# Kernel tuning notes

Hardware: AMD Instinct MI355X
Metric: run time of the kernel (lower is better)

## Reference

```python
import jax, jax.numpy as jnp
import numpy as np

B, S, D, H = 1, 2048, 1280, 16
HD = D // H  # 80


def setup_inputs() -> dict:
    key = jax.random.key(0)
    ks = jax.random.split(key, 6)
    return {
        "hidden_states": jax.random.normal(ks[0], (B, S, D), dtype=jnp.float32),
        "rotary_pos_emb": jax.random.normal(ks[1], (S, HD // 2), dtype=jnp.float32),
        "qkv_w": jax.random.normal(ks[2], (3 * D, D), dtype=jnp.float32) * 0.02,
        "qkv_b": jax.random.normal(ks[3], (3 * D,), dtype=jnp.float32) * 0.02,
        "proj_w": jax.random.normal(ks[4], (D, D), dtype=jnp.float32) * 0.02,
        "proj_b": jax.random.normal(ks[5], (D,), dtype=jnp.float32) * 0.02,
    }


def reference(hidden_states, rotary_pos_emb, qkv_w, qkv_b, proj_w, proj_b):
    b, s, d = hidden_states.shape
    h = H
    hd = d // h
    scaling = hd ** -0.5

    # fused QKV projection: [b, s, 3*d]
    qkv = hidden_states @ qkv_w.T + qkv_b
    qkv = qkv.reshape(b, s, 3, h, hd)
    q, k, v = qkv[:, :, 0], qkv[:, :, 1], qkv[:, :, 2]  # each [b, s, h, hd]

    # rotary embedding: cos/sin [s, hd//2] -> [1, s, 1, hd]
    cos = jnp.cos(rotary_pos_emb)
    sin = jnp.sin(rotary_pos_emb)
    cos = jnp.concatenate([cos, cos], axis=-1)[None, :, None, :]
    sin = jnp.concatenate([sin, sin], axis=-1)[None, :, None, :]

    def apply_rope(x):
        x1, x2 = x[..., : hd // 2], x[..., hd // 2:]
        return x * cos + jnp.concatenate([-x2, x1], axis=-1) * sin

    q = apply_rope(q)
    k = apply_rope(k)

    # [b, h, s, hd]
    q = q.transpose(0, 2, 1, 3)
    k = k.transpose(0, 2, 1, 3)
    v = v.transpose(0, 2, 1, 3)

    # naive full attention matrix [b, h, s, s]
    attn = jnp.einsum("bhqd,bhkd->bhqk", q, k) * scaling
    attn = jax.nn.softmax(attn, axis=-1)
    out = jnp.einsum("bhqk,bhkd->bhqd", attn, v)
    out = out.transpose(0, 2, 1, 3).reshape(b, s, d)
    return out @ proj_w.T + proj_b
```

## Files before the change

kernel.cpp:

```cpp
#include <hip/hip_runtime.h>
#include <math.h>

#define SS 2048
#define DD 1280
#define HH 16
#define HDD 80
#define ND3 3840

typedef __attribute__((ext_vector_type(8))) short short8;
typedef __attribute__((ext_vector_type(4))) short s16x4;
typedef __attribute__((ext_vector_type(4))) float f32x4;
typedef __attribute__((ext_vector_type(8))) _Float16 h16x8;
typedef __attribute__((ext_vector_type(4))) _Float16 h16x4;

__device__ inline short f2bf(float f) {
    union { float f; unsigned u; } x; x.f = f;
    unsigned r = x.u + 0x7FFF + ((x.u >> 16) & 1);
    return (short)(r >> 16);
}

__global__ __launch_bounds__(256) void split_f16(
    const float* __restrict__ a, _Float16* __restrict__ ah, int nbA,
    const float* __restrict__ b, _Float16* __restrict__ bh, int nbB,
    const float* __restrict__ c, _Float16* __restrict__ ch)
{
    const float* x; _Float16* h;
    int blk = blockIdx.x;
    if (blk < nbA)            { x = a; h = ah; }
    else if (blk < nbA + nbB) { blk -= nbA; x = b; h = bh; }
    else                      { blk -= nbA + nbB; x = c; h = ch; }
    int i = (blk * 256 + threadIdx.x) * 4;
    float4 v = *(const float4*)(x + i);
    h16x4 hv;
    hv[0] = (_Float16)v.x; hv[1] = (_Float16)v.y;
    hv[2] = (_Float16)v.z; hv[3] = (_Float16)v.w;
    *(h16x4*)(h + i) = hv;
}

#define LDSA(m, kg) ((m) * 32 + (((kg) ^ (((m) >> 1) & 3)) << 3))

template <int BMT, int BNT>
__global__ __launch_bounds__(256) void gemm_f16_sk(
    const _Float16* __restrict__ Ah, const _Float16* __restrict__ Bh,
    const float* __restrict__ bias, _Float16* __restrict__ Cp,
    int M, int N, int K, int Kh)
{
    constexpr int IT = BMT / 32;
    constexpr int JT = BNT / 32;
    constexpr int AU = BMT / 64;
    constexpr int BU = BNT / 64;
    __shared__ _Float16 AhS[BMT * 32];
    __shared__ _Float16 BhS[BNT * 32];

    const int tid = threadIdx.x;
    const int w = tid >> 6;
    const int lane = tid & 63;
    const int l15 = lane & 15;
    const int quad = lane >> 4;
    const int wm = w >> 1, wn = w & 1;
    const int bm = blockIdx.y * BMT;
    const int bn = blockIdx.x * BNT;
    const int z = blockIdx.z;
    const int kbeg = z * Kh, kend = kbeg + Kh;

    f32x4 acc[IT][JT];
    #pragma unroll
    for (int i = 0; i < IT; ++i)
        #pragma unroll
        for (int j = 0; j < JT; ++j)
            acc[i][j] = (f32x4){0.f, 0.f, 0.f, 0.f};

    h16x8 rah[AU], rbh[BU];
    auto loadg = [&](int k0) {
        #pragma unroll
        for (int u = 0; u < AU; ++u) {
            int c = tid + u * 256, m = c >> 2, kg = c & 3;
            rah[u] = *(const h16x8*)(Ah + (size_t)(bm + m) * K + k0 + kg * 8);
        }
        #pragma unroll
        for (int u = 0; u < BU; ++u) {
            int c = tid + u * 256, m = c >> 2, kg = c & 3;
            rbh[u] = *(const h16x8*)(Bh + (size_t)(bn + m) * K + k0 + kg * 8);
        }
    };

    loadg(kbeg);
    for (int k0 = kbeg; k0 < kend; k0 += 32) {
        __syncthreads();
        #pragma unroll
        for (int u = 0; u < AU; ++u) {
            int c = tid + u * 256, m = c >> 2, kg = c & 3;
            *(h16x8*)&AhS[LDSA(m, kg)] = rah[u];
        }
        #pragma unroll
        for (int u = 0; u < BU; ++u) {
            int c = tid + u * 256, m = c >> 2, kg = c & 3;
            *(h16x8*)&BhS[LDSA(m, kg)] = rbh[u];
        }
        __syncthreads();
        if (k0 + 32 < kend) loadg(k0 + 32);

        h16x8 af[IT], bf[JT];
        #pragma unroll
        for (int i = 0; i < IT; ++i) {
            int m = wm * (BMT / 2) + i * 16 + l15;
            af[i] = *(h16x8*)&AhS[LDSA(m, quad)];
        }
        #pragma unroll
        for (int j = 0; j < JT; ++j) {
            int n = wn * (BNT / 2) + j * 16 + l15;
            bf[j] = *(h16x8*)&BhS[LDSA(n, quad)];
        }
        #pragma unroll
        for (int i = 0; i < IT; ++i)
            #pragma unroll
            for (int j = 0; j < JT; ++j)
                acc[i][j] = __builtin_amdgcn_mfma_f32_16x16x32_f16(af[i], bf[j], acc[i][j], 0, 0, 0);
    }

    _Float16* C = Cp + (size_t)z * M * N;
    #pragma unroll
    for (int j = 0; j < JT; ++j) {
        int col = bn + wn * (BNT / 2) + j * 16 + l15;
        float bb = (z == 0) ? bias[col] : 0.f;
        #pragma unroll
        for (int i = 0; i < IT; ++i)
            #pragma unroll
            for (int r = 0; r < 4; ++r) {
                int row = bm + wm * (BMT / 2) + i * 16 + quad * 4 + r;
                C[(size_t)row * N + col] = (_Float16)(acc[i][j][r] + bb);
            }
    }
}

template <int BMT, int BNT>
__global__ __launch_bounds__(256) void gemm_f16(
    const _Float16* __restrict__ Ah, const _Float16* __restrict__ Bh,
    const float* __restrict__ bias, float* __restrict__ C,
    int M, int N, int K)
{
    constexpr int IT = BMT / 32;
    constexpr int JT = BNT / 32;
    constexpr int AU = BMT / 64;
    constexpr int BU = BNT / 64;
    __shared__ _Float16 AhS[BMT * 32];
    __shared__ _Float16 BhS[BNT * 32];

    const int tid = threadIdx.x;
    const int w = tid >> 6;
    const int lane = tid & 63;
    const int l15 = lane & 15;
    const int quad = lane >> 4;
    const int wm = w >> 1, wn = w & 1;
    const int bm = blockIdx.y * BMT;
    const int bn = blockIdx.x * BNT;

    f32x4 acc[IT][JT];
    #pragma unroll
    for (int i = 0; i < IT; ++i)
        #pragma unroll
        for (int j = 0; j < JT; ++j)
            acc[i][j] = (f32x4){0.f, 0.f, 0.f, 0.f};

    h16x8 rah[AU], rbh[BU];
    auto loadg = [&](int k0) {
        #pragma unroll
        for (int u = 0; u < AU; ++u) {
            int c = tid + u * 256, m = c >> 2, kg = c & 3;
            rah[u] = *(const h16x8*)(Ah + (size_t)(bm + m) * K + k0 + kg * 8);
        }
        #pragma unroll
        for (int u = 0; u < BU; ++u) {
            int c = tid + u * 256, m = c >> 2, kg = c & 3;
            rbh[u] = *(const h16x8*)(Bh + (size_t)(bn + m) * K + k0 + kg * 8);
        }
    };

    loadg(0);
    for (int k0 = 0; k0 < K; k0 += 32) {
        __syncthreads();
        #pragma unroll
        for (int u = 0; u < AU; ++u) {
            int c = tid + u * 256, m = c >> 2, kg = c & 3;
            *(h16x8*)&AhS[LDSA(m, kg)] = rah[u];
        }
        #pragma unroll
        for (int u = 0; u < BU; ++u) {
            int c = tid + u * 256, m = c >> 2, kg = c & 3;
            *(h16x8*)&BhS[LDSA(m, kg)] = rbh[u];
        }
        __syncthreads();
        if (k0 + 32 < K) loadg(k0 + 32);

        h16x8 af[IT], bf[JT];
        #pragma unroll
        for (int i = 0; i < IT; ++i) {
            int m = wm * (BMT / 2) + i * 16 + l15;
            af[i] = *(h16x8*)&AhS[LDSA(m, quad)];
        }
        #pragma unroll
        for (int j = 0; j < JT; ++j) {
            int n = wn * (BNT / 2) + j * 16 + l15;
            bf[j] = *(h16x8*)&BhS[LDSA(n, quad)];
        }
        #pragma unroll
        for (int i = 0; i < IT; ++i)
            #pragma unroll
            for (int j = 0; j < JT; ++j)
                acc[i][j] = __builtin_amdgcn_mfma_f32_16x16x32_f16(af[i], bf[j], acc[i][j], 0, 0, 0);
    }

    #pragma unroll
    for (int j = 0; j < JT; ++j) {
        int col = bn + wn * (BNT / 2) + j * 16 + l15;
        float bb = bias[col];
        #pragma unroll
        for (int i = 0; i < IT; ++i)
            #pragma unroll
            for (int r = 0; r < 4; ++r) {
                int row = bm + wm * (BMT / 2) + i * 16 + quad * 4 + r;
                C[(size_t)row * N + col] = acc[i][j][r] + bb;
            }
    }
}

__global__ __launch_bounds__(256) void rope_scatter_bf16(
    const _Float16* __restrict__ p0, const _Float16* __restrict__ p1,
    const float* __restrict__ rpe,
    short* __restrict__ q, short* __restrict__ k, short* __restrict__ v)
{
    __shared__ float cs[40], sn[40];
    const int s = blockIdx.x;
    if (threadIdx.x < 40)
        __sincosf(rpe[s * 40 + threadIdx.x], &sn[threadIdx.x], &cs[threadIdx.x]);
    __syncthreads();
    const float scale = 0.11180339887498949f;
    for (int j = threadIdx.x; j < ND3; j += 256) {
        int p = j / DD;
        int rem = j - p * DD;
        int hh = rem / HDD;
        int d = rem - hh * HDD;
        size_t base = (size_t)s * ND3;
        float x = (float)p0[base + j] + (float)p1[base + j];
        float val;
        if (p == 2) {
            val = x;
        } else {
            int dm = (d < 40) ? d : d - 40;
            size_t oi = base + p * DD + hh * HDD + ((d < 40) ? d + 40 : d - 40);
            float oth = (float)p0[oi] + (float)p1[oi];
            if (d < 40) oth = -oth;
            val = x * cs[dm] + oth * sn[dm];
            if (p == 0) val *= scale;
        }
        short* dst = (p == 0) ? q : (p == 1) ? k : v;
        dst[((size_t)hh * SS + s) * HDD + d] = f2bf(val);
    }
}

__global__ __launch_bounds__(256) void attn_mfma(
    const short* __restrict__ q, const short* __restrict__ k,
    const short* __restrict__ v, _Float16* __restrict__ o_part,
    float* __restrict__ l_part)
{
    __shared__ short Ks[64][88];
    __shared__ short Vts[80 * 64];
    __shared__ short Ps[4][32][72];

    const int h = blockIdx.y;
    const int q0 = blockIdx.x << 7;
    const int z = blockIdx.z;
    const int tid = threadIdx.x;
    const int w = tid >> 6;
    const int lane = tid & 63;
    const int l15 = lane & 15;
    const int quad = lane >> 4;

    const short* qbase = q + (size_t)h * SS * HDD;
    const short* kbase = k + (size_t)h * SS * HDD;
    const short* vbase = v + (size_t)h * SS * HDD;

    short8 qf[2][3];
    #pragma unroll
    for (int i = 0; i < 2; ++i) {
        const int row = q0 + w * 32 + i * 16 + l15;
        qf[i][0] = *(const short8*)(qbase + (size_t)row * HDD + quad * 8);
        qf[i][1] = *(const short8*)(qbase + (size_t)row * HDD + 32 + quad * 8);
        qf[i][2] = (quad < 2) ? *(const short8*)(qbase + (size_t)row * HDD + 64 + quad * 8)
                              : (short8)0;
    }

    if (tid < 64)
        *(short8*)&Ks[tid][80] = (short8)0;

    float lsum[2][4] = {{0.f}};
    f32x4 o[2][5];
    #pragma unroll
    for (int i = 0; i < 2; ++i)
        #pragma unroll
        for (int n = 0; n < 5; ++n) o[i][n] = (f32x4){0.f, 0.f, 0.f, 0.f};

    const int kt0 = z << 9;
    for (int kt = kt0; kt < kt0 + 512; kt += 64) {
        __syncthreads();
        #pragma unroll
        for (int u = 0; u < 3; ++u) {
            int i = tid + u * 256;
            if (i < 640) {
                int r = i / 10, c = (i - r * 10) * 8;
                *(short8*)&Ks[r][c] = *(const short8*)(kbase + (size_t)(kt + r) * HDD + c);
            }
        }
        #pragma unroll
        for (int u = 0; u < 2; ++u) {
            int task = tid + u * 256;
            if (task < 320) {
                int r4 = (task & 15) << 2;
                int d4 = (task >> 4) << 2;
                s16x4 a0 = *(const s16x4*)(vbase + (size_t)(kt + r4 + 0) * HDD + d4);
                s16x4 a1 = *(const s16x4*)(vbase + (size_t)(kt + r4 + 1) * HDD + d4);
                s16x4 a2 = *(const s16x4*)(vbase + (size_t)(kt + r4 + 2) * HDD + d4);
                s16x4 a3 = *(const s16x4*)(vbase + (size_t)(kt + r4 + 3) * HDD + d4);
                #pragma unroll
                for (int j = 0; j < 4; ++j) {
                    s16x4 w4 = {a0[j], a1[j], a2[j], a3[j]};
                    int d = d4 + j;
                    int sw = (r4 >> 3) ^ (d & 7);
                    *(s16x4*)&Vts[d * 64 + sw * 8 + (r4 & 7)] = w4;
                }
            }
        }
        __syncthreads();

        f32x4 s_[2][4];
        #pragma unroll
        for (int nt = 0; nt < 4; ++nt) {
            short8 bf0 = *(short8*)&Ks[nt * 16 + l15][quad * 8];
            short8 bf1 = *(short8*)&Ks[nt * 16 + l15][32 + quad * 8];
            short8 bf2 = *(short8*)&Ks[nt * 16 + l15][64 + quad * 8];
            #pragma unroll
            for (int i = 0; i < 2; ++i) {
                f32x4 acc = (f32x4){0.f, 0.f, 0.f, 0.f};
                acc = __builtin_amdgcn_mfma_f32_16x16x32_bf16(qf[i][0], bf0, acc, 0, 0, 0);
                acc = __builtin_amdgcn_mfma_f32_16x16x32_bf16(qf[i][1], bf1, acc, 0, 0, 0);
                acc = __builtin_amdgcn_mfma_f32_16x16x32_bf16(qf[i][2], bf2, acc, 0, 0, 0);
                s_[i][nt] = acc;
            }
        }

        #pragma unroll
        for (int i = 0; i < 2; ++i)
            #pragma unroll
            for (int nt = 0; nt < 4; ++nt)
                #pragma unroll
                for (int r = 0; r < 4; ++r) {
                    float p = __expf(s_[i][nt][r] - 8.f);
                    lsum[i][r] += p;
                    Ps[w][i * 16 + quad * 4 + r][nt * 16 + l15] = f2bf(p);
                }

        short8 pf[2][2];
        #pragma unroll
        for (int i = 0; i < 2; ++i)
            #pragma unroll
            for (int kk = 0; kk < 2; ++kk)
                pf[i][kk] = *(short8*)&Ps[w][i * 16 + l15][kk * 32 + quad * 8];
        #pragma unroll
        for (int n = 0; n < 5; ++n) {
            #pragma unroll
            for (int kk = 0; kk < 2; ++kk) {
                int d = n * 16 + l15;
                int sw = (kk * 4 + quad) ^ (l15 & 7);
                short8 vf = *(short8*)&Vts[d * 64 + sw * 8];
                #pragma unroll
                for (int i = 0; i < 2; ++i)
                    o[i][n] = __builtin_amdgcn_mfma_f32_16x16x32_bf16(pf[i][kk], vf, o[i][n], 0, 0, 0);
            }
        }
    }

    _Float16* ob = o_part + (size_t)z * SS * DD;
    #pragma unroll
    for (int i = 0; i < 2; ++i) {
        #pragma unroll
        for (int r = 0; r < 4; ++r) {
            float rs = lsum[i][r];
            #pragma unroll
            for (int off = 1; off < 16; off <<= 1)
                rs += __shfl_xor(rs, off, 64);
            lsum[i][r] = rs;
        }
        #pragma unroll
        for (int n = 0; n < 5; ++n)
            #pragma unroll
            for (int r = 0; r < 4; ++r) {
                int row = q0 + w * 32 + i * 16 + quad * 4 + r;
                ob[(size_t)row * DD + h * HDD + n * 16 + l15] = (_Float16)o[i][n][r];
            }
        if (l15 == 0)
            #pragma unroll
            for (int r = 0; r < 4; ++r)
                l_part[((size_t)z * HH + h) * SS + q0 + w * 32 + i * 16 + quad * 4 + r] = lsum[i][r];
    }
}

__global__ __launch_bounds__(256) void attn_merge(
    const _Float16* __restrict__ o_part, const float* __restrict__ l_part,
    _Float16* __restrict__ oh)
{
    int i = (blockIdx.x * 256 + threadIdx.x) * 4;
    int row = i / DD;
    int col = i - row * DD;
    int h = col / HDD;
    float l = 0.f;
    float acc[4] = {0.f, 0.f, 0.f, 0.f};
    #pragma unroll
    for (int zz = 0; zz < 4; ++zz) {
        l += l_part[(zz * HH + h) * SS + row];
        h16x4 a = *(const h16x4*)(o_part + (size_t)zz * SS * DD + i);
        acc[0] += (float)a[0]; acc[1] += (float)a[1];
        acc[2] += (float)a[2]; acc[3] += (float)a[3];
    }
    float inv = 1.f / l;
    h16x4 hv;
    hv[0] = (_Float16)(acc[0] * inv);
    hv[1] = (_Float16)(acc[1] * inv);
    hv[2] = (_Float16)(acc[2] * inv);
    hv[3] = (_Float16)(acc[3] * inv);
    *(h16x4*)(oh + i) = hv;
}

extern "C" void kernel_launch(void* const* d_in, const int* in_sizes, int n_in,
                              void* d_out, int out_size, void* d_ws, size_t ws_size,
                              hipStream_t stream)
{
    const float* hs     = (const float*)d_in[0];
    const float* rpe    = (const float*)d_in[1];
    const float* qkv_w  = (const float*)d_in[2];
    const float* qkv_b  = (const float*)d_in[3];
    const float* proj_w = (const float*)d_in[4];
    const float* proj_b = (const float*)d_in[5];
    float* out = (float*)d_out;

    short* s0 = (short*)d_ws;
    _Float16* qkv_p = (_Float16*)s0;
    _Float16* o_part = (_Float16*)s0;
    float* l_part = (float*)(s0 + 10485760);
    short* s1 = s0 + 15728640;
    _Float16* qkvw_h = (_Float16*)s1;
    short* qb = s1;
    short* kb = s1 + 2621440;
    short* vb = s1 + 5242880;
    _Float16* attn_h = (_Float16*)s1;
    short* s2 = s1 + 7864320;
    _Float16* hs_h = (_Float16*)s2;
    _Float16* projw_h = (_Float16*)s2;

    const int n_hs = SS * DD;
    const int n_qw = ND3 * DD;
    const int n_pw = DD * DD;

    split_f16<<<n_hs / 1024 + n_qw / 1024, 256, 0, stream>>>(
        hs, hs_h, n_hs / 1024,
        qkv_w, qkvw_h, n_qw / 1024,
        qkv_w, qkvw_h);
    gemm_f16_sk<128, 128><<<dim3(ND3 / 128, SS / 128, 2), 256, 0, stream>>>(
        hs_h, qkvw_h, qkv_b, qkv_p, SS, ND3, DD, DD / 2);
    split_f16<<<n_pw / 1024, 256, 0, stream>>>(
        proj_w, projw_h, n_pw / 1024,
        proj_w, projw_h, 0,
        proj_w, projw_h);
    rope_scatter_bf16<<<SS, 256, 0, stream>>>(
        qkv_p, qkv_p + (size_t)SS * ND3, rpe, qb, kb, vb);
    attn_mfma<<<dim3(SS / 128, HH, 4), 256, 0, stream>>>(qb, kb, vb, o_part, l_part);
    attn_merge<<<(SS * DD) / 1024, 256, 0, stream>>>(o_part, l_part, attn_h);
    gemm_f16<64, 128><<<dim3(DD / 128, SS / 64), 256, 0, stream>>>(
        attn_h, projw_h, proj_b, out, SS, DD, DD);
}
```

Baseline: 228.9 us.

## Fuse attention merge into projection GEMM and drop QKV split-K

The QKV GEMM runs without split-K and writes fp32 output directly, so the rope kernel reads one buffer instead of summing two fp16 partials. The rope kernel is vectorised to process four elements per thread. Attention key splits drop from 4 to 2, and the separate merge kernel is folded into the projection GEMM, which sums the two partials and normalises by 1/l while staging A tiles. The proj_w conversion joins the first split launch. Together these remove two launches and an intermediate buffer round trip, at the cost of less parallelism in the QKV GEMM and attention grids.

```diff
diff --git a/kernel.cpp b/kernel.cpp
--- a/kernel.cpp
+++ b/kernel.cpp
@@ -40,10 +40,10 @@
 #define LDSA(m, kg) ((m) * 32 + (((kg) ^ (((m) >> 1) & 3)) << 3))
 
 template <int BMT, int BNT>
-__global__ __launch_bounds__(256) void gemm_f16_sk(
+__global__ __launch_bounds__(256) void gemm_f16(
     const _Float16* __restrict__ Ah, const _Float16* __restrict__ Bh,
-    const float* __restrict__ bias, _Float16* __restrict__ Cp,
-    int M, int N, int K, int Kh)
+    const float* __restrict__ bias, float* __restrict__ C,
+    int M, int N, int K)
 {
     constexpr int IT = BMT / 32;
     constexpr int JT = BNT / 32;
@@ -60,8 +60,6 @@
     const int wm = w >> 1, wn = w & 1;
     const int bm = blockIdx.y * BMT;
     const int bn = blockIdx.x * BNT;
-    const int z = blockIdx.z;
-    const int kbeg = z * Kh, kend = kbeg + Kh;
 
     f32x4 acc[IT][JT];
     #pragma unroll
@@ -84,8 +82,8 @@
         }
     };
 
-    loadg(kbeg);
-    for (int k0 = kbeg; k0 < kend; k0 += 32) {
+    loadg(0);
+    for (int k0 = 0; k0 < K; k0 += 32) {
         __syncthreads();
         #pragma unroll
         for (int u = 0; u < AU; ++u) {
@@ -98,7 +96,7 @@
             *(h16x8*)&BhS[LDSA(m, kg)] = rbh[u];
         }
         __syncthreads();
-        if (k0 + 32 < kend) loadg(k0 + 32);
+        if (k0 + 32 < K) loadg(k0 + 32);
 
         h16x8 af[IT], bf[JT];
         #pragma unroll
@@ -118,33 +116,32 @@
                 acc[i][j] = __builtin_amdgcn_mfma_f32_16x16x32_f16(af[i], bf[j], acc[i][j], 0, 0, 0);
     }
 
-    _Float16* C = Cp + (size_t)z * M * N;
     #pragma unroll
     for (int j = 0; j < JT; ++j) {
         int col = bn + wn * (BNT / 2) + j * 16 + l15;
-        float bb = (z == 0) ? bias[col] : 0.f;
+        float bb = bias[col];
         #pragma unroll
         for (int i = 0; i < IT; ++i)
             #pragma unroll
             for (int r = 0; r < 4; ++r) {
                 int row = bm + wm * (BMT / 2) + i * 16 + quad * 4 + r;
-                C[(size_t)row * N + col] = (_Float16)(acc[i][j][r] + bb);
-            }
-    }
-}
-
-template <int BMT, int BNT>
-__global__ __launch_bounds__(256) void gemm_f16(
-    const _Float16* __restrict__ Ah, const _Float16* __restrict__ Bh,
+                C[(size_t)row * N + col] = acc[i][j][r] + bb;
+            }
+    }
+}
+
+__global__ __launch_bounds__(256) void gemm_proj_merge(
+    const _Float16* __restrict__ o_part, const float* __restrict__ l_part,
+    const _Float16* __restrict__ Bh,
     const float* __restrict__ bias, float* __restrict__ C,
     int M, int N, int K)
 {
-    constexpr int IT = BMT / 32;
+    constexpr int BMT = 64, BNT = 128;
     constexpr int JT = BNT / 32;
-    constexpr int AU = BMT / 64;
     constexpr int BU = BNT / 64;
     __shared__ _Float16 AhS[BMT * 32];
     __shared__ _Float16 BhS[BNT * 32];
+    __shared__ float linvS[HH * 64];
 
     const int tid = threadIdx.x;
     const int w = tid >> 6;
@@ -155,19 +152,27 @@
     const int bm = blockIdx.y * BMT;
     const int bn = blockIdx.x * BNT;
 
-    f32x4 acc[IT][JT];
-    #pragma unroll
-    for (int i = 0; i < IT; ++i)
+    for (int i = tid; i < HH * 64; i += 256) {
+        int h = i >> 6, r = i & 63;
+        float l0 = l_part[(size_t)h * SS + bm + r];
+        float l1 = l_part[(size_t)(HH + h) * SS + bm + r];
+        linvS[i] = 1.f / (l0 + l1);
+    }
+
+    f32x4 acc[2][JT];
+    #pragma unroll
+    for (int i = 0; i < 2; ++i)
         #pragma unroll
         for (int j = 0; j < JT; ++j)
             acc[i][j] = (f32x4){0.f, 0.f, 0.f, 0.f};
 
-    h16x8 rah[AU], rbh[BU];
+    h16x8 ra0, ra1, rbh[BU];
     auto loadg = [&](int k0) {
-        #pragma unroll
-        for (int u = 0; u < AU; ++u) {
-            int c = tid + u * 256, m = c >> 2, kg = c & 3;
-            rah[u] = *(const h16x8*)(Ah + (size_t)(bm + m) * K + k0 + kg * 8);
+        {
+            int m = tid >> 2, kg = tid & 3;
+            size_t off = (size_t)(bm + m) * K + k0 + kg * 8;
+            ra0 = *(const h16x8*)(o_part + off);
+            ra1 = *(const h16x8*)(o_part + (size_t)SS * DD + off);
         }
         #pragma unroll
         for (int u = 0; u < BU; ++u) {
@@ -179,10 +184,16 @@
     loadg(0);
     for (int k0 = 0; k0 < K; k0 += 32) {
         __syncthreads();
-        #pragma unroll
-        for (int u = 0; u < AU; ++u) {
-            int c = tid + u * 256, m = c >> 2, kg = c & 3;
-            *(h16x8*)&AhS[LDSA(m, kg)] = rah[u];
+        {
+            int m = tid >> 2, kg = tid & 3;
+            int koff = k0 + kg * 8;
+            int h = koff / HDD;
+            float inv = linvS[h * 64 + m];
+            h16x8 f;
+            #pragma unroll
+            for (int e = 0; e < 8; ++e)
+                f[e] = (_Float16)(((float)ra0[e] + (float)ra1[e]) * inv);
+            *(h16x8*)&AhS[LDSA(m, kg)] = f;
         }
         #pragma unroll
         for (int u = 0; u < BU; ++u) {
@@ -192,19 +203,19 @@
         __syncthreads();
         if (k0 + 32 < K) loadg(k0 + 32);
 
-        h16x8 af[IT], bf[JT];
-        #pragma unroll
-        for (int i = 0; i < IT; ++i) {
-            int m = wm * (BMT / 2) + i * 16 + l15;
+        h16x8 af[2], bf[JT];
+        #pragma unroll
+        for (int i = 0; i < 2; ++i) {
+            int m = wm * 32 + i * 16 + l15;
             af[i] = *(h16x8*)&AhS[LDSA(m, quad)];
         }
         #pragma unroll
         for (int j = 0; j < JT; ++j) {
-            int n = wn * (BNT / 2) + j * 16 + l15;
+            int n = wn * 64 + j * 16 + l15;
             bf[j] = *(h16x8*)&BhS[LDSA(n, quad)];
         }
         #pragma unroll
-        for (int i = 0; i < IT; ++i)
+        for (int i = 0; i < 2; ++i)
             #pragma unroll
             for (int j = 0; j < JT; ++j)
                 acc[i][j] = __builtin_amdgcn_mfma_f32_16x16x32_f16(af[i], bf[j], acc[i][j], 0, 0, 0);
@@ -212,49 +223,57 @@
 
     #pragma unroll
     for (int j = 0; j < JT; ++j) {
-        int col = bn + wn * (BNT / 2) + j * 16 + l15;
+        int col = bn + wn * 64 + j * 16 + l15;
         float bb = bias[col];
         #pragma unroll
-        for (int i = 0; i < IT; ++i)
+        for (int i = 0; i < 2; ++i)
             #pragma unroll
             for (int r = 0; r < 4; ++r) {
-                int row = bm + wm * (BMT / 2) + i * 16 + quad * 4 + r;
+                int row = bm + wm * 32 + i * 16 + quad * 4 + r;
                 C[(size_t)row * N + col] = acc[i][j][r] + bb;
             }
     }
 }
 
 __global__ __launch_bounds__(256) void rope_scatter_bf16(
-    const _Float16* __restrict__ p0, const _Float16* __restrict__ p1,
-    const float* __restrict__ rpe,
+    const float* __restrict__ qkv, const float* __restrict__ rpe,
     short* __restrict__ q, short* __restrict__ k, short* __restrict__ v)
 {
-    __shared__ float cs[40], sn[40];
+    __shared__ __align__(16) float cs[40], sn[40];
     const int s = blockIdx.x;
     if (threadIdx.x < 40)
         __sincosf(rpe[s * 40 + threadIdx.x], &sn[threadIdx.x], &cs[threadIdx.x]);
     __syncthreads();
     const float scale = 0.11180339887498949f;
-    for (int j = threadIdx.x; j < ND3; j += 256) {
-        int p = j / DD;
-        int rem = j - p * DD;
+    const float* src = qkv + (size_t)s * ND3;
+    for (int t = threadIdx.x; t < ND3 / 4; t += 256) {
+        int j4 = t * 4;
+        int p = j4 / DD;
+        int rem = j4 - p * DD;
         int hh = rem / HDD;
         int d = rem - hh * HDD;
-        size_t base = (size_t)s * ND3;
-        float x = (float)p0[base + j] + (float)p1[base + j];
-        float val;
+        float4 x = *(const float4*)(src + j4);
+        float vv[4];
         if (p == 2) {
-            val = x;
+            vv[0] = x.x; vv[1] = x.y; vv[2] = x.z; vv[3] = x.w;
         } else {
-            int dm = (d < 40) ? d : d - 40;
-            size_t oi = base + p * DD + hh * HDD + ((d < 40) ? d + 40 : d - 40);
-            float oth = (float)p0[oi] + (float)p1[oi];
-            if (d < 40) oth = -oth;
-            val = x * cs[dm] + oth * sn[dm];
-            if (p == 0) val *= scale;
+            bool lo = d < 40;
+            int dm = lo ? d : d - 40;
+            float4 oth = *(const float4*)(src + p * DD + hh * HDD + (lo ? d + 40 : d - 40));
+            float4 c4 = *(const float4*)&cs[dm];
+            float4 s4 = *(const float4*)&sn[dm];
+            float sg = lo ? -1.f : 1.f;
+            vv[0] = x.x * c4.x + sg * oth.x * s4.x;
+            vv[1] = x.y * c4.y + sg * oth.y * s4.y;
+            vv[2] = x.z * c4.z + sg * oth.z * s4.z;
+            vv[3] = x.w * c4.w + sg * oth.w * s4.w;
+            if (p == 0) { vv[0] *= scale; vv[1] *= scale; vv[2] *= scale; vv[3] *= scale; }
         }
         short* dst = (p == 0) ? q : (p == 1) ? k : v;
-        dst[((size_t)hh * SS + s) * HDD + d] = f2bf(val);
+        s16x4 o4;
+        o4[0] = f2bf(vv[0]); o4[1] = f2bf(vv[1]);
+        o4[2] = f2bf(vv[2]); o4[3] = f2bf(vv[3]);
+        *(s16x4*)(dst + ((size_t)hh * SS + s) * HDD + d) = o4;
     }
 }
 
@@ -263,7 +282,7 @@
     const short* __restrict__ v, _Float16* __restrict__ o_part,
     float* __restrict__ l_part)
 {
-    __shared__ short Ks[64][88];
+    __shared__ short Ks[64][104];
     __shared__ short Vts[80 * 64];
     __shared__ short Ps[4][32][72];
 
@@ -284,14 +303,18 @@
     #pragma unroll
     for (int i = 0; i < 2; ++i) {
         const int row = q0 + w * 32 + i * 16 + l15;
-        qf[i][0] = *(const short8*)(qbase + (size_t)row * HDD + quad * 8);
-        qf[i][1] = *(const short8*)(qbase + (size_t)row * HDD + 32 + quad * 8);
-        qf[i][2] = (quad < 2) ? *(const short8*)(qbase + (size_t)row * HDD + 64 + quad * 8)
-                              : (short8)0;
-    }
-
-    if (tid < 64)
-        *(short8*)&Ks[tid][80] = (short8)0;
+        #pragma unroll
+        for (int kk = 0; kk < 3; ++kk) {
+            int c0 = kk * 32 + quad * 8;
+            qf[i][kk] = (c0 < HDD) ? *(const short8*)(qbase + (size_t)row * HDD + c0)
+                                   : (short8)0;
+        }
+    }
+
+    if (tid < 128) {
+        int r = tid >> 1, c = 80 + (tid & 1) * 8;
+        *(short8*)&Ks[r][c] = (short8)0;
+    }
 
     float lsum[2][4] = {{0.f}};
     f32x4 o[2][5];
@@ -300,8 +323,8 @@
         #pragma unroll
         for (int n = 0; n < 5; ++n) o[i][n] = (f32x4){0.f, 0.f, 0.f, 0.f};
 
-    const int kt0 = z << 9;
-    for (int kt = kt0; kt < kt0 + 512; kt += 64) {
+    const int kt0 = z << 10;
+    for (int kt = kt0; kt < kt0 + 1024; kt += 64) {
         __syncthreads();
         #pragma unroll
         for (int u = 0; u < 3; ++u) {
@@ -404,32 +427,6 @@
     }
 }
 
-__global__ __launch_bounds__(256) void attn_merge(
-    const _Float16* __restrict__ o_part, const float* __restrict__ l_part,
-    _Float16* __restrict__ oh)
-{
-    int i = (blockIdx.x * 256 + threadIdx.x) * 4;
-    int row = i / DD;
-    int col = i - row * DD;
-    int h = col / HDD;
-    float l = 0.f;
-    float acc[4] = {0.f, 0.f, 0.f, 0.f};
-    #pragma unroll
-    for (int zz = 0; zz < 4; ++zz) {
-        l += l_part[(zz * HH + h) * SS + row];
-        h16x4 a = *(const h16x4*)(o_part + (size_t)zz * SS * DD + i);
-        acc[0] += (float)a[0]; acc[1] += (float)a[1];
-        acc[2] += (float)a[2]; acc[3] += (float)a[3];
-    }
-    float inv = 1.f / l;
-    h16x4 hv;
-    hv[0] = (_Float16)(acc[0] * inv);
-    hv[1] = (_Float16)(acc[1] * inv);
-    hv[2] = (_Float16)(acc[2] * inv);
-    hv[3] = (_Float16)(acc[3] * inv);
-    *(h16x4*)(oh + i) = hv;
-}
-
 extern "C" void kernel_launch(void* const* d_in, const int* in_sizes, int n_in,
                               void* d_out, int out_size, void* d_ws, size_t ws_size,
                               hipStream_t stream)
@@ -443,7 +440,7 @@
     float* out = (float*)d_out;
 
     short* s0 = (short*)d_ws;
-    _Float16* qkv_p = (_Float16*)s0;
+    float* qkv_f  = (float*)d_ws;
     _Float16* o_part = (_Float16*)s0;
     float* l_part = (float*)(s0 + 10485760);
     short* s1 = s0 + 15728640;
@@ -451,29 +448,23 @@
     short* qb = s1;
     short* kb = s1 + 2621440;
     short* vb = s1 + 5242880;
-    _Float16* attn_h = (_Float16*)s1;
     short* s2 = s1 + 7864320;
     _Float16* hs_h = (_Float16*)s2;
-    _Float16* projw_h = (_Float16*)s2;
+    short* s3 = s2 + 2621440;
+    _Float16* projw_h = (_Float16*)s3;
 
     const int n_hs = SS * DD;
     const int n_qw = ND3 * DD;
     const int n_pw = DD * DD;
 
-    split_f16<<<n_hs / 1024 + n_qw / 1024, 256, 0, stream>>>(
+    split_f16<<<n_hs / 1024 + n_qw / 1024 + n_pw / 1024, 256, 0, stream>>>(
         hs, hs_h, n_hs / 1024,
         qkv_w, qkvw_h, n_qw / 1024,
-        qkv_w, qkvw_h);
-    gemm_f16_sk<128, 128><<<dim3(ND3 / 128, SS / 128, 2), 256, 0, stream>>>(
-        hs_h, qkvw_h, qkv_b, qkv_p, SS, ND3, DD, DD / 2);
-    split_f16<<<n_pw / 1024, 256, 0, stream>>>(
-        proj_w, projw_h, n_pw / 1024,
-        proj_w, projw_h, 0,
         proj_w, projw_h);
-    rope_scatter_bf16<<<SS, 256, 0, stream>>>(
-        qkv_p, qkv_p + (size_t)SS * ND3, rpe, qb, kb, vb);
-    attn_mfma<<<dim3(SS / 128, HH, 4), 256, 0, stream>>>(qb, kb, vb, o_part, l_part);
-    attn_merge<<<(SS * DD) / 1024, 256, 0, stream>>>(o_part, l_part, attn_h);
-    gemm_f16<64, 128><<<dim3(DD / 128, SS / 64), 256, 0, stream>>>(
-        attn_h, projw_h, proj_b, out, SS, DD, DD);
-}
+    gemm_f16<128, 128><<<dim3(ND3 / 128, SS / 128), 256, 0, stream>>>(
+        hs_h, qkvw_h, qkv_b, qkv_f, SS, ND3, DD);
+    rope_scatter_bf16<<<SS, 256, 0, stream>>>(qkv_f, rpe, qb, kb, vb);
+    attn_mfma<<<dim3(SS / 128, HH, 2), 256, 0, stream>>>(qb, kb, vb, o_part, l_part);
+    gemm_proj_merge<<<dim3(DD / 128, SS / 64), 256, 0, stream>>>(
+        o_part, l_part, projw_h, proj_b, out, SS, DD, DD);
+}
```

Result: faster. 211.8 us (-7.5%).
